# Kernel tuning notes

Hardware: AMD Instinct MI355X
Metric: run time of the kernel (lower is better)

Reference implementation:

```python
import jax, jax.numpy as jnp
import numpy as np
from jax import lax

VOCAB, VEC, HID, L, BATCH, OPT, K = 50000, 256, 256, 256, 8, 4, 2
H2, H8 = 2 * HID, 8 * HID


def _gru_dir(x, wih, whh, bih, bhh, reverse):
    # x: [B, L, D]; PyTorch GRU cell math.
    B = x.shape[0]
    H = whh.shape[1]
    def step(h, xt):
        gi = xt @ wih.T + bih            # [B, 3H]
        gh = h @ whh.T + bhh             # [B, 3H]
        ir, iz, inn = jnp.split(gi, 3, axis=-1)
        hr, hz, hn = jnp.split(gh, 3, axis=-1)
        r = jax.nn.sigmoid(ir + hr)
        z = jax.nn.sigmoid(iz + hz)
        n = jnp.tanh(inn + r * hn)
        hnew = (1.0 - z) * n + z * h
        return hnew, hnew
    h0 = jnp.zeros((B, H), x.dtype)
    _, ys = lax.scan(step, h0, jnp.swapaxes(x, 0, 1), reverse=reverse)
    return jnp.swapaxes(ys, 0, 1)        # [B, L, H]


def _bigru(x, wih, whh, bih, bhh):
    f = _gru_dir(x, wih[0], whh[0], bih[0], bhh[0], False)
    b = _gru_dir(x, wih[1], whh[1], bih[1], bhh[1], True)
    return jnp.concatenate([f, b], axis=-1)


def _bidaf(c, q, w, b):
    # s[b,i,j] = w_c.c_i + w_q.q_j + sum_d c_id*q_jd*w_cq_d + (b_c+b_q+b_cq)
    s = (c @ w[0])[:, :, None] + (q @ w[1])[:, None, :] \
        + jnp.einsum('bcd,bqd->bcq', c * w[2], q) + (b[0] + b[1] + b[2])
    a = jax.nn.softmax(s, axis=2)
    c2q = jnp.einsum('bcq,bqd->bcd', a, q)
    bb = jax.nn.softmax(jnp.max(s, axis=2), axis=1)        # [B, c_len]
    q2c = jnp.einsum('bc,bcd->bd', bb, c)[:, None, :]       # [B, 1, D]
    return jnp.concatenate([c, c2q, c * c2q, c * q2c], axis=-1)


def setup_inputs() -> dict:
    key = jax.random.key(0)
    ks = jax.random.split(key, 20)
    s = 0.05
    return {
        'question': jax.random.randint(ks[0], (BATCH, OPT, L), 0, VOCAB),
        'article': jax.random.randint(ks[1], (BATCH, OPT * K, L), 0, VOCAB),
        'emb': jax.random.normal(ks[2], (VOCAB, VEC), jnp.float32),
        'g1_wih': jax.random.normal(ks[3], (2, 3 * HID, VEC), jnp.float32) * s,
        'g1_whh': jax.random.normal(ks[4], (2, 3 * HID, HID), jnp.float32) * s,
        'g1_bih': jax.random.normal(ks[5], (2, 3 * HID), jnp.float32) * s,
        'g1_bhh': jax.random.normal(ks[6], (2, 3 * HID), jnp.float32) * s,
        'g2_wih': jax.random.normal(ks[7], (2, 3 * HID, H8), jnp.float32) * s,
        'g2_whh': jax.random.normal(ks[8], (2, 3 * HID, HID), jnp.float32) * s,
        'g2_bih': jax.random.normal(ks[9], (2, 3 * HID), jnp.float32) * s,
        'g2_bhh': jax.random.normal(ks[10], (2, 3 * HID), jnp.float32) * s,
        'b1_w': jax.random.normal(ks[11], (3, H2), jnp.float32) * s,
        'b1_b': jax.random.normal(ks[12], (3,), jnp.float32) * s,
        'b2_w': jax.random.normal(ks[13], (3, H2), jnp.float32) * s,
        'b2_b': jax.random.normal(ks[14], (3,), jnp.float32) * s,
        'rank_w': jax.random.normal(ks[15], (H8 * L,), jnp.float32) * 0.002,
        'rank_b': jax.random.normal(ks[16], (1,), jnp.float32) * s,
        'k': K,
        'option': OPT,
    }


def reference(question, article, emb, g1_wih, g1_whh, g1_bih, g1_bhh,
              g2_wih, g2_whh, g2_bih, g2_bhh, b1_w, b1_b, b2_w, b2_b,
              rank_w, rank_b, k, option):
    batch, _, max_len = question.shape
    # question.repeat(1,1,k).view(B*opt*k, L)
    q_ids = jnp.tile(question, (1, 1, k)).reshape(batch * option * k, max_len)
    a_ids = article.reshape(batch * option * k, max_len)
    qx = emb[q_ids]                                  # [Beff, L, VEC]
    ax = emb[a_ids]
    qh = _bigru(qx, g1_wih, g1_whh, g1_bih, g1_bhh)  # shared encoder, [Beff, L, 2H]
    ah = _bigru(ax, g1_wih, g1_whh, g1_bih, g1_bhh)
    att = jax.nn.relu(_bidaf(qh, ah, b1_w, b1_b))    # [Beff, L, 8H]
    ax2 = _bigru(att, g2_wih, g2_whh, g2_bih, g2_bhh)  # [Beff, L, 2H]
    ax2 = jax.nn.relu(_bidaf(ax2, ax2, b2_w, b2_b))    # [Beff, L, 8H]
    s = att + ax2
    # rank_method == 'max': max over k copies, then linear
    y = s.reshape(batch * option, k, -1)
    y = jnp.max(y, axis=1)                           # [B*opt, L*8H]
    y = y @ rank_w + rank_b[0]                       # [B*opt]
    return y.reshape(batch, option)
```

## Files before the change

### kernel.cpp

```cpp
#include <hip/hip_runtime.h>
#include <math.h>

#define LSEQ 256
#define HID 256
#define H2 512
#define H3 768
#define H8 2048

typedef __attribute__((ext_vector_type(8))) short short8;
typedef __attribute__((ext_vector_type(4))) float floatx4;

__device__ __forceinline__ unsigned short f2bf(float f) {
    unsigned int u = __float_as_uint(f);
    u = (u + 0x7FFFu + ((u >> 16) & 1u)) >> 16;
    return (unsigned short)u;
}
__device__ __forceinline__ float bf2f(unsigned short h) {
    return __uint_as_float(((unsigned int)h) << 16);
}
__device__ __forceinline__ float fsig(float x) {
    return __builtin_amdgcn_rcpf(1.f + __expf(-x));
}
__device__ __forceinline__ float ftanh(float x) {
    return __builtin_fmaf(2.f, __builtin_amdgcn_rcpf(1.f + __expf(-2.f * x)), -1.f);
}
__device__ __forceinline__ void bfsplit(float x, unsigned short& hi, unsigned short& lo) {
    hi = f2bf(x);
    lo = f2bf(x - bf2f(hi));
}

__global__ void embed_kernel(const int* __restrict__ question,
                             const int* __restrict__ article,
                             const float* __restrict__ emb,
                             unsigned short* __restrict__ xemb) {
    int gid = blockIdx.x * 256 + threadIdx.x;
    int d = gid & 255;
    int rl = gid >> 8;
    int l = rl & 255;
    int stream = rl >> 8;
    int id;
    if (stream < 64) {
        int b = stream >> 3, o = (stream & 7) >> 1;
        id = question[(b * 4 + o) * 256 + l];
    } else {
        id = article[(stream - 64) * 256 + l];
    }
    xemb[(size_t)gid] = f2bf(emb[(size_t)id * 256 + d]);
}

__global__ void pack_bf8(const float* __restrict__ src, unsigned short* __restrict__ dst, int n8) {
    int i = blockIdx.x * 256 + threadIdx.x;
    if (i >= n8) return;
    float4 a = ((const float4*)src)[2 * i];
    float4 b = ((const float4*)src)[2 * i + 1];
    uint4 o;
    o.x = (unsigned int)f2bf(a.x) | ((unsigned int)f2bf(a.y) << 16);
    o.y = (unsigned int)f2bf(a.z) | ((unsigned int)f2bf(a.w) << 16);
    o.z = (unsigned int)f2bf(b.x) | ((unsigned int)f2bf(b.y) << 16);
    o.w = (unsigned int)f2bf(b.z) | ((unsigned int)f2bf(b.w) << 16);
    ((uint4*)dst)[i] = o;
}

__global__ __launch_bounds__(256)
void gemm_a16b16(const unsigned short* __restrict__ A, const unsigned short* __restrict__ B,
                 const float* __restrict__ bias, unsigned short* __restrict__ C,
                 int M, int N, int K) {
    __shared__ unsigned short At[128][40];
    __shared__ unsigned short Bt[128][40];
    int tid = threadIdx.x;
    int m0 = blockIdx.x * 128, n0 = blockIdx.y * 128;
    int l = tid & 63, w = tid >> 6;
    int wm = (w & 1) * 64, wn = (w >> 1) * 64;
    int lr = l & 15, koff = (l >> 4) * 8;
    int srow = tid >> 1, scol = (tid & 1) * 16;
    floatx4 acc[4][4];
#pragma unroll
    for (int i = 0; i < 4; i++)
#pragma unroll
        for (int j = 0; j < 4; j++) acc[i][j] = (floatx4){0.f, 0.f, 0.f, 0.f};
    for (int k0 = 0; k0 < K; k0 += 32) {
        const unsigned short* ap = A + (size_t)(m0 + srow) * K + k0 + scol;
        const unsigned short* bp = B + (size_t)(n0 + srow) * K + k0 + scol;
        uint4 a0 = *(const uint4*)(ap);
        uint4 a1 = *(const uint4*)(ap + 8);
        uint4 b0 = *(const uint4*)(bp);
        uint4 b1 = *(const uint4*)(bp + 8);
        __syncthreads();
        *(uint4*)&At[srow][scol]     = a0;
        *(uint4*)&At[srow][scol + 8] = a1;
        *(uint4*)&Bt[srow][scol]     = b0;
        *(uint4*)&Bt[srow][scol + 8] = b1;
        __syncthreads();
        short8 af[4], bf[4];
#pragma unroll
        for (int i = 0; i < 4; i++) {
            af[i] = *(const short8*)&At[wm + i * 16 + lr][koff];
            bf[i] = *(const short8*)&Bt[wn + i * 16 + lr][koff];
        }
#pragma unroll
        for (int i = 0; i < 4; i++)
#pragma unroll
            for (int j = 0; j < 4; j++)
                acc[i][j] = __builtin_amdgcn_mfma_f32_16x16x32_bf16(af[i], bf[j], acc[i][j], 0, 0, 0);
    }
    int quad = l >> 4;
#pragma unroll
    for (int i = 0; i < 4; i++) {
#pragma unroll
        for (int j = 0; j < 4; j++) {
            int n = n0 + wn + j * 16 + lr;
            float bs = bias[n];
#pragma unroll
            for (int r = 0; r < 4; r++) {
                int m = m0 + wm + i * 16 + quad * 4 + r;
                C[(size_t)m * N + n] = f2bf(acc[i][j][r] + bs);
            }
        }
    }
}

__global__ __launch_bounds__(256)
void gemm_a32b16(const float* __restrict__ A, const unsigned short* __restrict__ B,
                 const float* __restrict__ bias, unsigned short* __restrict__ C,
                 int M, int N, int K) {
    __shared__ unsigned short At[128][40];
    __shared__ unsigned short Bt[128][40];
    int tid = threadIdx.x;
    int m0 = blockIdx.x * 128, n0 = blockIdx.y * 128;
    int l = tid & 63, w = tid >> 6;
    int wm = (w & 1) * 64, wn = (w >> 1) * 64;
    int lr = l & 15, koff = (l >> 4) * 8;
    int srow = tid >> 1, scol = (tid & 1) * 16;
    floatx4 acc[4][4];
#pragma unroll
    for (int i = 0; i < 4; i++)
#pragma unroll
        for (int j = 0; j < 4; j++) acc[i][j] = (floatx4){0.f, 0.f, 0.f, 0.f};
    for (int k0 = 0; k0 < K; k0 += 32) {
        const float* ap = A + (size_t)(m0 + srow) * K + k0 + scol;
        const unsigned short* bp = B + (size_t)(n0 + srow) * K + k0 + scol;
        float av[16];
        *(float4*)&av[0]  = *(const float4*)(ap);
        *(float4*)&av[4]  = *(const float4*)(ap + 4);
        *(float4*)&av[8]  = *(const float4*)(ap + 8);
        *(float4*)&av[12] = *(const float4*)(ap + 12);
        uint4 b0 = *(const uint4*)(bp);
        uint4 b1 = *(const uint4*)(bp + 8);
        unsigned int aw[8];
#pragma unroll
        for (int i = 0; i < 8; i++)
            aw[i] = (unsigned int)f2bf(av[2 * i]) | ((unsigned int)f2bf(av[2 * i + 1]) << 16);
        __syncthreads();
        *(uint4*)&At[srow][scol]     = *(uint4*)&aw[0];
        *(uint4*)&At[srow][scol + 8] = *(uint4*)&aw[4];
        *(uint4*)&Bt[srow][scol]     = b0;
        *(uint4*)&Bt[srow][scol + 8] = b1;
        __syncthreads();
        short8 af[4], bf[4];
#pragma unroll
        for (int i = 0; i < 4; i++) {
            af[i] = *(const short8*)&At[wm + i * 16 + lr][koff];
            bf[i] = *(const short8*)&Bt[wn + i * 16 + lr][koff];
        }
#pragma unroll
        for (int i = 0; i < 4; i++)
#pragma unroll
            for (int j = 0; j < 4; j++)
                acc[i][j] = __builtin_amdgcn_mfma_f32_16x16x32_bf16(af[i], bf[j], acc[i][j], 0, 0, 0);
    }
    int quad = l >> 4;
#pragma unroll
    for (int i = 0; i < 4; i++) {
#pragma unroll
        for (int j = 0; j < 4; j++) {
            int n = n0 + wn + j * 16 + lr;
            float bs = bias[n];
#pragma unroll
            for (int r = 0; r < 4; r++) {
                int m = m0 + wm + i * 16 + quad * 4 + r;
                C[(size_t)m * N + n] = f2bf(acc[i][j][r] + bs);
            }
        }
    }
}

__global__ __launch_bounds__(512, 2)
void gru_scan_rreg(const unsigned short* __restrict__ gi_f,
                   const unsigned short* __restrict__ gi_b,
                   const unsigned short* __restrict__ whh_bf,
                   const float* __restrict__ bhh,
                   float* __restrict__ out) {
    int blk = blockIdx.x;
    int d = blk & 1, s = blk >> 1;
    const unsigned short* gi_blk = (d ? gi_b : gi_f) + (size_t)s * LSEQ * H3;
    const unsigned short* wb = whh_bf + (size_t)d * H3 * HID;

    __shared__ __align__(16) unsigned short h_pack[2][256];

    int tid = threadIdx.x;
    int lane = tid & 63, wave = tid >> 6;
    int lr = lane & 15, kq = lane >> 4;

    short8 bq[6][8];
#pragma unroll
    for (int nt = 0; nt < 6; nt++) {
        int row = (nt >> 1) * 256 + wave * 32 + (nt & 1) * 16 + lr;
        const unsigned short* wp = wb + (size_t)row * HID + kq * 8;
#pragma unroll
        for (int kt = 0; kt < 8; kt++)
            bq[nt][kt] = *(const short8*)(wp + kt * 32);
    }

    int hh0 = wave * 32 + lr, hh1 = hh0 + 16;
    float br0 = bhh[d * H3 + hh0],       br1 = bhh[d * H3 + hh1];
    float bz0 = bhh[d * H3 + 256 + hh0], bz1 = bhh[d * H3 + 256 + hh1];
    float bn0 = bhh[d * H3 + 512 + hh0], bn1 = bhh[d * H3 + 512 + hh1];

    int t0 = d ? (LSEQ - 1) : 0;
    int tstep = d ? -1 : 1;

    if (tid < 128) ((unsigned int*)h_pack[0])[tid] = 0;
    float hold0 = 0.f, hold1 = 0.f;

    unsigned short gr0, gz0, gn0, gr1, gz1, gn1;
    {
        const unsigned short* gp = gi_blk + (size_t)t0 * H3;
        gr0 = gp[hh0]; gz0 = gp[256 + hh0]; gn0 = gp[512 + hh0];
        gr1 = gp[hh1]; gz1 = gp[256 + hh1]; gn1 = gp[512 + hh1];
    }
    __syncthreads();

    int cur = 0, t = t0;
    for (int step = 0; step < LSEQ; ++step) {
        unsigned short nr0 = 0, nz0 = 0, nn0 = 0, nr1 = 0, nz1 = 0, nn1 = 0;
        if (step + 1 < LSEQ) {
            const unsigned short* gp = gi_blk + (size_t)(t + tstep) * H3;
            nr0 = gp[hh0]; nz0 = gp[256 + hh0]; nn0 = gp[512 + hh0];
            nr1 = gp[hh1]; nz1 = gp[256 + hh1]; nn1 = gp[512 + hh1];
        }
        floatx4 acc[6];
#pragma unroll
        for (int nt = 0; nt < 6; nt++) acc[nt] = (floatx4){0.f, 0.f, 0.f, 0.f};
#pragma unroll
        for (int kt = 0; kt < 8; kt++) {
            short8 av = *(const short8*)&h_pack[cur][kt * 32 + kq * 8];
#pragma unroll
            for (int nt = 0; nt < 6; nt++)
                acc[nt] = __builtin_amdgcn_mfma_f32_16x16x32_bf16(av, bq[nt][kt], acc[nt], 0, 0, 0);
        }
        float rg0 = fsig(bf2f(gr0) + acc[0][0] + br0);
        float rg1 = fsig(bf2f(gr1) + acc[1][0] + br1);
        float zg0 = fsig(bf2f(gz0) + acc[2][0] + bz0);
        float zg1 = fsig(bf2f(gz1) + acc[3][0] + bz1);
        float ng0 = ftanh(bf2f(gn0) + rg0 * (acc[4][0] + bn0));
        float ng1 = ftanh(bf2f(gn1) + rg1 * (acc[5][0] + bn1));
        float h0 = (1.f - zg0) * ng0 + zg0 * hold0;
        float h1 = (1.f - zg1) * ng1 + zg1 * hold1;
        hold0 = h0; hold1 = h1;
        int nxt = cur ^ 1;
        if (kq == 0) {
            h_pack[nxt][hh0] = f2bf(h0);
            h_pack[nxt][hh1] = f2bf(h1);
            float* op = out + ((size_t)s * LSEQ + t) * H2 + d * HID;
            op[hh0] = h0;
            op[hh1] = h1;
        }
        gr0 = nr0; gz0 = nz0; gn0 = nn0;
        gr1 = nr1; gz1 = nz1; gn1 = nn1;
        __syncthreads();
        cur = nxt; t += tstep;
    }
}

__global__ void cwqw_kernel(const float* __restrict__ c, const float* __restrict__ q,
                            const float* __restrict__ w,
                            float* __restrict__ cw, float* __restrict__ qw) {
    int row = blockIdx.x;
    int lane = threadIdx.x;
    const float* src; const float* wv; float* dst; int r;
    if (row < 16384) { src = c; wv = w; dst = cw; r = row; }
    else { src = q; wv = w + 512; dst = qw; r = row - 16384; }
    const float* p = src + (size_t)r * H2;
    float acc = 0.f;
    for (int j = lane; j < H2; j += 64) acc += p[j] * wv[j];
    for (int off = 32; off; off >>= 1) acc += __shfl_down(acc, off);
    if (lane == 0) dst[r] = acc;
}

__global__ __launch_bounds__(256)
void smat_mfma(const float* __restrict__ c, const float* __restrict__ q,
               const float* __restrict__ w2, const float* __restrict__ bvec,
               const float* __restrict__ cw, const float* __restrict__ qw,
               float* __restrict__ smat) {
    __shared__ __align__(16) unsigned short Ah[128][40];
    __shared__ __align__(16) unsigned short Al[128][40];
    __shared__ __align__(16) unsigned short Bh[128][40];
    __shared__ __align__(16) unsigned short Bl[128][40];
    int b = blockIdx.z;
    int m0 = blockIdx.x * 128, n0 = blockIdx.y * 128;
    int tid = threadIdx.x;
    int l = tid & 63, w = tid >> 6;
    int wm = (w & 1) * 64, wn = (w >> 1) * 64;
    int lr = l & 15, koff = (l >> 4) * 8;
    int srow = tid >> 1, scol = (tid & 1) * 16;
    floatx4 acc[4][4];
#pragma unroll
    for (int i = 0; i < 4; i++)
#pragma unroll
        for (int j = 0; j < 4; j++) acc[i][j] = (floatx4){0.f, 0.f, 0.f, 0.f};
    const float* ap0 = c + (size_t)(b * 256 + m0 + srow) * H2 + scol;
    const float* bp0 = q + (size_t)(b * 256 + n0 + srow) * H2 + scol;
    for (int k0 = 0; k0 < H2; k0 += 32) {
        float av[16], bv[16], wv[16];
        *(float4*)&av[0]  = *(const float4*)(ap0 + k0);
        *(float4*)&av[4]  = *(const float4*)(ap0 + k0 + 4);
        *(float4*)&av[8]  = *(const float4*)(ap0 + k0 + 8);
        *(float4*)&av[12] = *(const float4*)(ap0 + k0 + 12);
        *(float4*)&bv[0]  = *(const float4*)(bp0 + k0);
        *(float4*)&bv[4]  = *(const float4*)(bp0 + k0 + 4);
        *(float4*)&bv[8]  = *(const float4*)(bp0 + k0 + 8);
        *(float4*)&bv[12] = *(const float4*)(bp0 + k0 + 12);
        *(float4*)&wv[0]  = *(const float4*)(w2 + k0 + scol);
        *(float4*)&wv[4]  = *(const float4*)(w2 + k0 + scol + 4);
        *(float4*)&wv[8]  = *(const float4*)(w2 + k0 + scol + 8);
        *(float4*)&wv[12] = *(const float4*)(w2 + k0 + scol + 12);
        unsigned int ahw[8], alw[8], bhw[8], blw[8];
#pragma unroll
        for (int j = 0; j < 8; j++) {
            float p0 = av[2 * j] * wv[2 * j], p1 = av[2 * j + 1] * wv[2 * j + 1];
            unsigned short h0, s0, h1, s1;
            bfsplit(p0, h0, s0); bfsplit(p1, h1, s1);
            ahw[j] = (unsigned int)h0 | ((unsigned int)h1 << 16);
            alw[j] = (unsigned int)s0 | ((unsigned int)s1 << 16);
            unsigned short g0, t0, g1, t1;
            bfsplit(bv[2 * j], g0, t0); bfsplit(bv[2 * j + 1], g1, t1);
            bhw[j] = (unsigned int)g0 | ((unsigned int)g1 << 16);
            blw[j] = (unsigned int)t0 | ((unsigned int)t1 << 16);
        }
        __syncthreads();
        *(uint4*)&Ah[srow][scol]     = *(uint4*)&ahw[0];
        *(uint4*)&Ah[srow][scol + 8] = *(uint4*)&ahw[4];
        *(uint4*)&Al[srow][scol]     = *(uint4*)&alw[0];
        *(uint4*)&Al[srow][scol + 8] = *(uint4*)&alw[4];
        *(uint4*)&Bh[srow][scol]     = *(uint4*)&bhw[0];
        *(uint4*)&Bh[srow][scol + 8] = *(uint4*)&bhw[4];
        *(uint4*)&Bl[srow][scol]     = *(uint4*)&blw[0];
        *(uint4*)&Bl[srow][scol + 8] = *(uint4*)&blw[4];
        __syncthreads();
        short8 afh[4], afl[4], bfh[4], bfl[4];
#pragma unroll
        for (int i = 0; i < 4; i++) {
            afh[i] = *(const short8*)&Ah[wm + i * 16 + lr][koff];
            afl[i] = *(const short8*)&Al[wm + i * 16 + lr][koff];
            bfh[i] = *(const short8*)&Bh[wn + i * 16 + lr][koff];
            bfl[i] = *(const short8*)&Bl[wn + i * 16 + lr][koff];
        }
#pragma unroll
        for (int i = 0; i < 4; i++)
#pragma unroll
            for (int j = 0; j < 4; j++) {
                acc[i][j] = __builtin_amdgcn_mfma_f32_16x16x32_bf16(afl[i], bfh[j], acc[i][j], 0, 0, 0);
                acc[i][j] = __builtin_amdgcn_mfma_f32_16x16x32_bf16(afh[i], bfl[j], acc[i][j], 0, 0, 0);
                acc[i][j] = __builtin_amdgcn_mfma_f32_16x16x32_bf16(afh[i], bfh[j], acc[i][j], 0, 0, 0);
            }
    }
    float bsum = bvec[0] + bvec[1] + bvec[2];
    int quad = l >> 4;
#pragma unroll
    for (int i = 0; i < 4; i++) {
#pragma unroll
        for (int j = 0; j < 4; j++) {
            int n = n0 + wn + j * 16 + lr;
            float qwv = qw[b * 256 + n] + bsum;
#pragma unroll
            for (int r = 0; r < 4; r++) {
                int m = m0 + wm + i * 16 + quad * 4 + r;
                smat[((size_t)(b * 256 + m)) * 256 + n] = acc[i][j][r] + cw[b * 256 + m] + qwv;
            }
        }
    }
}

__global__ void softmax_kernel(float* __restrict__ smat, float* __restrict__ rowmax) {
    int row = blockIdx.x;
    int lane = threadIdx.x;
    float* p = smat + (size_t)row * LSEQ;
    float v[4];
    float mx = -1e30f;
#pragma unroll
    for (int j = 0; j < 4; j++) { v[j] = p[lane + j * 64]; mx = fmaxf(mx, v[j]); }
    for (int off = 32; off; off >>= 1) mx = fmaxf(mx, __shfl_down(mx, off));
    mx = __shfl(mx, 0);
    float sum = 0.f;
#pragma unroll
    for (int j = 0; j < 4; j++) { v[j] = __expf(v[j] - mx); sum += v[j]; }
    for (int off = 32; off; off >>= 1) sum += __shfl_down(sum, off);
    sum = __shfl(sum, 0);
    float inv = 1.f / sum;
#pragma unroll
    for (int j = 0; j < 4; j++) p[lane + j * 64] = v[j] * inv;
    if (lane == 0) rowmax[row] = mx;
}

__global__ void bb_kernel(const float* __restrict__ rowmax, float* __restrict__ bb) {
    int b = blockIdx.x; int t = threadIdx.x;
    __shared__ float red[256];
    float v = rowmax[b * LSEQ + t];
    red[t] = v; __syncthreads();
    for (int s = 128; s; s >>= 1) { if (t < s) red[t] = fmaxf(red[t], red[t + s]); __syncthreads(); }
    float mx = red[0]; __syncthreads();
    float e = __expf(v - mx);
    red[t] = e; __syncthreads();
    for (int s = 128; s; s >>= 1) { if (t < s) red[t] += red[t + s]; __syncthreads(); }
    bb[b * LSEQ + t] = e / red[0];
}

__global__ void q2c_kernel(const float* __restrict__ bb, const float* __restrict__ c,
                           float* __restrict__ q2c) {
    int b = blockIdx.x;
    int d = blockIdx.y * 128 + threadIdx.x;
    const float* cb = c + (size_t)b * LSEQ * H2 + d;
    const float* bbp = bb + b * LSEQ;
    float a0 = 0.f, a1 = 0.f, a2 = 0.f, a3 = 0.f;
    for (int i = 0; i < LSEQ; i += 4) {
        a0 += bbp[i]     * cb[(size_t)i * H2];
        a1 += bbp[i + 1] * cb[(size_t)(i + 1) * H2];
        a2 += bbp[i + 2] * cb[(size_t)(i + 2) * H2];
        a3 += bbp[i + 3] * cb[(size_t)(i + 3) * H2];
    }
    q2c[b * H2 + d] = (a0 + a1) + (a2 + a3);
}

__global__ __launch_bounds__(256)
void c2q_mfma(const float* __restrict__ amat, const float* __restrict__ q,
              const float* __restrict__ c, float* __restrict__ att, int add) {
    __shared__ __align__(16) unsigned short Ah[128][40];
    __shared__ __align__(16) unsigned short Al[128][40];
    __shared__ __align__(16) unsigned short Bh[128][40];
    __shared__ __align__(16) unsigned short Bl[128][40];
    int b = blockIdx.z;
    int m0 = blockIdx.x * 128, n0 = blockIdx.y * 128;
    int tid = threadIdx.x;
    int l = tid & 63, w = tid >> 6;
    int wm = (w & 1) * 64, wn = (w >> 1) * 64;
    int lr = l & 15, koff = (l >> 4) * 8;
    int srow = tid >> 1, scol = (tid & 1) * 16;
    int bn = tid & 127, bkh = tid >> 7;
    floatx4 acc[4][4];
#pragma unroll
    for (int i = 0; i < 4; i++)
#pragma unroll
        for (int j = 0; j < 4; j++) acc[i][j] = (floatx4){0.f, 0.f, 0.f, 0.f};
    for (int k0 = 0; k0 < LSEQ; k0 += 32) {
        float av[16];
        const float* ap = amat + (size_t)(b * 256 + m0 + srow) * 256 + k0 + scol;
        *(float4*)&av[0]  = *(const float4*)(ap);
        *(float4*)&av[4]  = *(const float4*)(ap + 4);
        *(float4*)&av[8]  = *(const float4*)(ap + 8);
        *(float4*)&av[12] = *(const float4*)(ap + 12);
        float qv[16];
        const float* qp = q + (size_t)(b * 256 + k0 + bkh * 16) * H2 + n0 + bn;
#pragma unroll
        for (int j = 0; j < 16; j++) qv[j] = qp[(size_t)j * H2];
        unsigned int ahw[8], alw[8], bhw[8], blw[8];
#pragma unroll
        for (int j = 0; j < 8; j++) {
            unsigned short h0, s0, h1, s1;
            bfsplit(av[2 * j], h0, s0); bfsplit(av[2 * j + 1], h1, s1);
            ahw[j] = (unsigned int)h0 | ((unsigned int)h1 << 16);
            alw[j] = (unsigned int)s0 | ((unsigned int)s1 << 16);
            unsigned short g0, t0, g1, t1;
            bfsplit(qv[2 * j], g0, t0); bfsplit(qv[2 * j + 1], g1, t1);
            bhw[j] = (unsigned int)g0 | ((unsigned int)g1 << 16);
            blw[j] = (unsigned int)t0 | ((unsigned int)t1 << 16);
        }
        __syncthreads();
        *(uint4*)&Ah[srow][scol]         = *(uint4*)&ahw[0];
        *(uint4*)&Ah[srow][scol + 8]     = *(uint4*)&ahw[4];
        *(uint4*)&Al[srow][scol]         = *(uint4*)&alw[0];
        *(uint4*)&Al[srow][scol + 8]     = *(uint4*)&alw[4];
        *(uint4*)&Bh[bn][bkh * 16]       = *(uint4*)&bhw[0];
        *(uint4*)&Bh[bn][bkh * 16 + 8]   = *(uint4*)&bhw[4];
        *(uint4*)&Bl[bn][bkh * 16]       = *(uint4*)&blw[0];
        *(uint4*)&Bl[bn][bkh * 16 + 8]   = *(uint4*)&blw[4];
        __syncthreads();
        short8 afh[4], afl[4], bfh[4], bfl[4];
#pragma unroll
        for (int i = 0; i < 4; i++) {
            afh[i] = *(const short8*)&Ah[wm + i * 16 + lr][koff];
            afl[i] = *(const short8*)&Al[wm + i * 16 + lr][koff];
            bfh[i] = *(const short8*)&Bh[wn + i * 16 + lr][koff];
            bfl[i] = *(const short8*)&Bl[wn + i * 16 + lr][koff];
        }
#pragma unroll
        for (int i = 0; i < 4; i++)
#pragma unroll
            for (int j = 0; j < 4; j++) {
                acc[i][j] = __builtin_amdgcn_mfma_f32_16x16x32_bf16(afl[i], bfh[j], acc[i][j], 0, 0, 0);
                acc[i][j] = __builtin_amdgcn_mfma_f32_16x16x32_bf16(afh[i], bfl[j], acc[i][j], 0, 0, 0);
                acc[i][j] = __builtin_amdgcn_mfma_f32_16x16x32_bf16(afh[i], bfh[j], acc[i][j], 0, 0, 0);
            }
    }
    int quad = l >> 4;
#pragma unroll
    for (int i = 0; i < 4; i++) {
#pragma unroll
        for (int j = 0; j < 4; j++) {
            int n = n0 + wn + j * 16 + lr;
#pragma unroll
            for (int r = 0; r < 4; r++) {
                int m = m0 + wm + i * 16 + quad * 4 + r;
                size_t row = (size_t)b * 256 + m;
                float a = acc[i][j][r];
                float cv = c[row * H2 + n];
                float v1 = fmaxf(a, 0.f);
                float v2 = fmaxf(cv * a, 0.f);
                float* p1 = att + row * H8 + 512 + n;
                float* p2 = att + row * H8 + 1024 + n;
                if (add) { *p1 += v1; *p2 += v2; }
                else     { *p1 = v1;  *p2 = v2; }
            }
        }
    }
}

__global__ void fixup03(const float* __restrict__ c, const float* __restrict__ q2c,
                        float* __restrict__ att, int add) {
    int row = blockIdx.x;
    int t = threadIdx.x;
    int b = row >> 8;
    float* o = att + (size_t)row * H8;
#pragma unroll
    for (int rep = 0; rep < 2; rep++) {
        int d = t + rep * 256;
        float cv = c[(size_t)row * H2 + d];
        float qv = q2c[b * H2 + d];
        float v0 = fmaxf(cv, 0.f);
        float v3 = fmaxf(cv * qv, 0.f);
        if (add) { o[d] += v0; o[d + 1536] += v3; }
        else     { o[d]  = v0; o[d + 1536]  = v3; }
    }
}

__global__ void reduce1_kernel(const float* __restrict__ s, const float* __restrict__ rw,
                               float* __restrict__ part) {
    int bo = blockIdx.x;
    int p = blockIdx.y;
    int t = threadIdx.x;
    const float* s0 = s + (size_t)(2 * bo) * 524288;
    const float* s1 = s0 + 524288;
    size_t base = (size_t)p * 65536;
    float acc = 0.f;
    for (int j = t; j < 65536; j += 256) {
        size_t m = base + j;
        acc += rw[m] * fmaxf(s0[m], s1[m]);
    }
    __shared__ float red[256];
    red[t] = acc; __syncthreads();
    for (int ss = 128; ss; ss >>= 1) { if (t < ss) red[t] += red[t + ss]; __syncthreads(); }
    if (t == 0) part[bo * 8 + p] = red[0];
}

__global__ void reduce2_kernel(const float* __restrict__ part, const float* __restrict__ rb,
                               float* __restrict__ out) {
    int t = threadIdx.x;
    float a = rb[0];
    for (int p = 0; p < 8; p++) a += part[t * 8 + p];
    out[t] = a;
}

extern "C" void kernel_launch(void* const* d_in, const int* in_sizes, int n_in,
                              void* d_out, int out_size, void* d_ws, size_t ws_size,
                              hipStream_t stream) {
    const int* question = (const int*)d_in[0];
    const int* article  = (const int*)d_in[1];
    const float* emb    = (const float*)d_in[2];
    const float* g1_wih = (const float*)d_in[3];
    const float* g1_whh = (const float*)d_in[4];
    const float* g1_bih = (const float*)d_in[5];
    const float* g1_bhh = (const float*)d_in[6];
    const float* g2_wih = (const float*)d_in[7];
    const float* g2_whh = (const float*)d_in[8];
    const float* g2_bih = (const float*)d_in[9];
    const float* g2_bhh = (const float*)d_in[10];
    const float* b1_w   = (const float*)d_in[11];
    const float* b1_b   = (const float*)d_in[12];
    const float* b2_w   = (const float*)d_in[13];
    const float* b2_b   = (const float*)d_in[14];
    const float* rank_w = (const float*)d_in[15];
    const float* rank_b = (const float*)d_in[16];
    float* ws = (float*)d_ws;
    float* out = (float*)d_out;

    unsigned short* WPK1  = (unsigned short*)(ws);
    unsigned short* WIH1B = (unsigned short*)(ws + 196608);
    unsigned short* WPK2  = (unsigned short*)(ws + 393216);
    unsigned short* WIH2B = (unsigned short*)(ws + 589824);
    float* CW   = ws + 2162688;
    float* QW   = ws + 2179072;
    float* RM   = ws + 2195456;
    float* BBv  = ws + 2211840;
    float* Q2C  = ws + 2228224;
    float* PART = ws + 2260992;
    unsigned short* XEMBB = (unsigned short*)(ws + 2293760);
    float*          SMAT  = ws + 2293760;
    unsigned short* GI2B  = (unsigned short*)(ws + 2293760);
    float*          HBUF  = ws + 6488064;
    float*          AX2   = ws + 14876672;
    float*          ATT   = ws + 25165824;
    unsigned short* GI1B  = (unsigned short*)(ws + 25165824);

    embed_kernel<<<32768, 256, 0, stream>>>(question, article, emb, XEMBB);
    pack_bf8<<<192, 256, 0, stream>>>(g1_whh, WPK1, 49152);
    pack_bf8<<<192, 256, 0, stream>>>(g1_wih, WIH1B, 49152);
    pack_bf8<<<192, 256, 0, stream>>>(g2_whh, WPK2, 49152);
    pack_bf8<<<1536, 256, 0, stream>>>(g2_wih, WIH2B, 393216);

    for (int d = 0; d < 2; d++) {
        gemm_a16b16<<<dim3(256, 6), 256, 0, stream>>>(
            XEMBB, WIH1B + (size_t)d * 196608, g1_bih + d * 768,
            GI1B + (size_t)d * 25165824, 32768, 768, 256);
    }
    gru_scan_rreg<<<256, 512, 0, stream>>>(GI1B, GI1B + (size_t)25165824, WPK1, g1_bhh, HBUF);

    float* QH = HBUF;
    float* AH = HBUF + (size_t)64 * 256 * 512;

    {
        cwqw_kernel<<<32768, 64, 0, stream>>>(QH, AH, b1_w, CW, QW);
        smat_mfma<<<dim3(2, 2, 64), 256, 0, stream>>>(QH, AH, b1_w + 1024, b1_b, CW, QW, SMAT);
        softmax_kernel<<<16384, 64, 0, stream>>>(SMAT, RM);
        bb_kernel<<<64, 256, 0, stream>>>(RM, BBv);
        q2c_kernel<<<dim3(64, 4), 128, 0, stream>>>(BBv, QH, Q2C);
        fixup03<<<16384, 256, 0, stream>>>(QH, Q2C, ATT, 0);
        c2q_mfma<<<dim3(2, 4, 64), 256, 0, stream>>>(SMAT, AH, QH, ATT, 0);
    }

    for (int d = 0; d < 2; d++) {
        gemm_a32b16<<<dim3(128, 6), 256, 0, stream>>>(
            ATT, WIH2B + (size_t)d * 1572864, g2_bih + d * 768,
            GI2B + (size_t)d * 12582912, 16384, 768, 2048);
    }
    gru_scan_rreg<<<128, 512, 0, stream>>>(GI2B, GI2B + (size_t)12582912, WPK2, g2_bhh, AX2);

    {
        cwqw_kernel<<<32768, 64, 0, stream>>>(AX2, AX2, b2_w, CW, QW);
        smat_mfma<<<dim3(2, 2, 64), 256, 0, stream>>>(AX2, AX2, b2_w + 1024, b2_b, CW, QW, SMAT);
        softmax_kernel<<<16384, 64, 0, stream>>>(SMAT, RM);
        bb_kernel<<<64, 256, 0, stream>>>(RM, BBv);
        q2c_kernel<<<dim3(64, 4), 128, 0, stream>>>(BBv, AX2, Q2C);
        fixup03<<<16384, 256, 0, stream>>>(AX2, Q2C, ATT, 1);
        c2q_mfma<<<dim3(2, 4, 64), 256, 0, stream>>>(SMAT, AX2, AX2, ATT, 1);
    }

    reduce1_kernel<<<dim3(32, 8), 256, 0, stream>>>(ATT, rank_w, PART);
    reduce2_kernel<<<1, 32, 0, stream>>>(PART, rank_b, out);
}
```

Before: 1.399 ms.

## Merge direction GEMMs, fuse fixup into c2q epilogue, pre-pack ATT to bf16

```diff
diff --git a/kernel.cpp b/kernel.cpp
--- a/kernel.cpp
+++ b/kernel.cpp
@@ -62,9 +62,9 @@
 }
 
 __global__ __launch_bounds__(256)
-void gemm_a16b16(const unsigned short* __restrict__ A, const unsigned short* __restrict__ B,
-                 const float* __restrict__ bias, unsigned short* __restrict__ C,
-                 int M, int N, int K) {
+void gemm_2dir(const unsigned short* __restrict__ A, const unsigned short* __restrict__ B,
+               const float* __restrict__ bias, unsigned short* __restrict__ C0,
+               unsigned short* __restrict__ C1, int mbase, int K) {
     __shared__ unsigned short At[128][40];
     __shared__ unsigned short Bt[128][40];
     int tid = threadIdx.x;
@@ -110,75 +110,12 @@
         for (int j = 0; j < 4; j++) {
             int n = n0 + wn + j * 16 + lr;
             float bs = bias[n];
+            unsigned short* dst = (n < 768) ? C0 : C1;
+            int nn = (n < 768) ? n : n - 768;
 #pragma unroll
             for (int r = 0; r < 4; r++) {
-                int m = m0 + wm + i * 16 + quad * 4 + r;
-                C[(size_t)m * N + n] = f2bf(acc[i][j][r] + bs);
-            }
-        }
-    }
-}
-
-__global__ __launch_bounds__(256)
-void gemm_a32b16(const float* __restrict__ A, const unsigned short* __restrict__ B,
-                 const float* __restrict__ bias, unsigned short* __restrict__ C,
-                 int M, int N, int K) {
-    __shared__ unsigned short At[128][40];
-    __shared__ unsigned short Bt[128][40];
-    int tid = threadIdx.x;
-    int m0 = blockIdx.x * 128, n0 = blockIdx.y * 128;
-    int l = tid & 63, w = tid >> 6;
-    int wm = (w & 1) * 64, wn = (w >> 1) * 64;
-    int lr = l & 15, koff = (l >> 4) * 8;
-    int srow = tid >> 1, scol = (tid & 1) * 16;
-    floatx4 acc[4][4];
-#pragma unroll
-    for (int i = 0; i < 4; i++)
-#pragma unroll
-        for (int j = 0; j < 4; j++) acc[i][j] = (floatx4){0.f, 0.f, 0.f, 0.f};
-    for (int k0 = 0; k0 < K; k0 += 32) {
-        const float* ap = A + (size_t)(m0 + srow) * K + k0 + scol;
-        const unsigned short* bp = B + (size_t)(n0 + srow) * K + k0 + scol;
-        float av[16];
-        *(float4*)&av[0]  = *(const float4*)(ap);
-        *(float4*)&av[4]  = *(const float4*)(ap + 4);
-        *(float4*)&av[8]  = *(const float4*)(ap + 8);
-        *(float4*)&av[12] = *(const float4*)(ap + 12);
-        uint4 b0 = *(const uint4*)(bp);
-        uint4 b1 = *(const uint4*)(bp + 8);
-        unsigned int aw[8];
-#pragma unroll
-        for (int i = 0; i < 8; i++)
-            aw[i] = (unsigned int)f2bf(av[2 * i]) | ((unsigned int)f2bf(av[2 * i + 1]) << 16);
-        __syncthreads();
-        *(uint4*)&At[srow][scol]     = *(uint4*)&aw[0];
-        *(uint4*)&At[srow][scol + 8] = *(uint4*)&aw[4];
-        *(uint4*)&Bt[srow][scol]     = b0;
-        *(uint4*)&Bt[srow][scol + 8] = b1;
-        __syncthreads();
-        short8 af[4], bf[4];
-#pragma unroll
-        for (int i = 0; i < 4; i++) {
-            af[i] = *(const short8*)&At[wm + i * 16 + lr][koff];
-            bf[i] = *(const short8*)&Bt[wn + i * 16 + lr][koff];
-        }
-#pragma unroll
-        for (int i = 0; i < 4; i++)
-#pragma unroll
-            for (int j = 0; j < 4; j++)
-                acc[i][j] = __builtin_amdgcn_mfma_f32_16x16x32_bf16(af[i], bf[j], acc[i][j], 0, 0, 0);
-    }
-    int quad = l >> 4;
-#pragma unroll
-    for (int i = 0; i < 4; i++) {
-#pragma unroll
-        for (int j = 0; j < 4; j++) {
-            int n = n0 + wn + j * 16 + lr;
-            float bs = bias[n];
-#pragma unroll
-            for (int r = 0; r < 4; r++) {
-                int m = m0 + wm + i * 16 + quad * 4 + r;
-                C[(size_t)m * N + n] = f2bf(acc[i][j][r] + bs);
+                int m = mbase + m0 + wm + i * 16 + quad * 4 + r;
+                dst[(size_t)m * 768 + nn] = f2bf(acc[i][j][r] + bs);
             }
         }
     }
@@ -432,8 +369,9 @@
 }
 
 __global__ __launch_bounds__(256)
-void c2q_mfma(const float* __restrict__ amat, const float* __restrict__ q,
-              const float* __restrict__ c, float* __restrict__ att, int add) {
+void c2q_fix_mfma(const float* __restrict__ amat, const float* __restrict__ q,
+                  const float* __restrict__ c, const float* __restrict__ q2c,
+                  float* __restrict__ att, int add) {
     __shared__ __align__(16) unsigned short Ah[128][40];
     __shared__ __align__(16) unsigned short Al[128][40];
     __shared__ __align__(16) unsigned short Bh[128][40];
@@ -507,38 +445,25 @@
 #pragma unroll
         for (int j = 0; j < 4; j++) {
             int n = n0 + wn + j * 16 + lr;
+            float q2cv = q2c[b * H2 + n];
 #pragma unroll
             for (int r = 0; r < 4; r++) {
                 int m = m0 + wm + i * 16 + quad * 4 + r;
                 size_t row = (size_t)b * 256 + m;
                 float a = acc[i][j][r];
                 float cv = c[row * H2 + n];
+                float v0 = fmaxf(cv, 0.f);
                 float v1 = fmaxf(a, 0.f);
                 float v2 = fmaxf(cv * a, 0.f);
-                float* p1 = att + row * H8 + 512 + n;
-                float* p2 = att + row * H8 + 1024 + n;
-                if (add) { *p1 += v1; *p2 += v2; }
-                else     { *p1 = v1;  *p2 = v2; }
+                float v3 = fmaxf(cv * q2cv, 0.f);
+                float* p0 = att + row * H8 + n;
+                float* p1 = p0 + 512;
+                float* p2 = p0 + 1024;
+                float* p3 = p0 + 1536;
+                if (add) { *p0 += v0; *p1 += v1; *p2 += v2; *p3 += v3; }
+                else     { *p0 = v0;  *p1 = v1;  *p2 = v2;  *p3 = v3; }
             }
         }
-    }
-}
-
-__global__ void fixup03(const float* __restrict__ c, const float* __restrict__ q2c,
-                        float* __restrict__ att, int add) {
-    int row = blockIdx.x;
-    int t = threadIdx.x;
-    int b = row >> 8;
-    float* o = att + (size_t)row * H8;
-#pragma unroll
-    for (int rep = 0; rep < 2; rep++) {
-        int d = t + rep * 256;
-        float cv = c[(size_t)row * H2 + d];
-        float qv = q2c[b * H2 + d];
-        float v0 = fmaxf(cv, 0.f);
-        float v3 = fmaxf(cv * qv, 0.f);
-        if (add) { o[d] += v0; o[d + 1536] += v3; }
-        else     { o[d]  = v0; o[d + 1536]  = v3; }
     }
 }
 
@@ -606,6 +531,7 @@
     float*          SMAT  = ws + 2293760;
     unsigned short* GI2B  = (unsigned short*)(ws + 2293760);
     float*          HBUF  = ws + 6488064;
+    unsigned short* ATTBH = (unsigned short*)(ws + 14876672);
     float*          AX2   = ws + 14876672;
     float*          ATT   = ws + 25165824;
     unsigned short* GI1B  = (unsigned short*)(ws + 25165824);
@@ -616,11 +542,8 @@
     pack_bf8<<<192, 256, 0, stream>>>(g2_whh, WPK2, 49152);
     pack_bf8<<<1536, 256, 0, stream>>>(g2_wih, WIH2B, 393216);
 
-    for (int d = 0; d < 2; d++) {
-        gemm_a16b16<<<dim3(256, 6), 256, 0, stream>>>(
-            XEMBB, WIH1B + (size_t)d * 196608, g1_bih + d * 768,
-            GI1B + (size_t)d * 25165824, 32768, 768, 256);
-    }
+    gemm_2dir<<<dim3(256, 12), 256, 0, stream>>>(
+        XEMBB, WIH1B, g1_bih, GI1B, GI1B + (size_t)25165824, 0, 256);
     gru_scan_rreg<<<256, 512, 0, stream>>>(GI1B, GI1B + (size_t)25165824, WPK1, g1_bhh, HBUF);
 
     float* QH = HBUF;
@@ -632,14 +555,13 @@
         softmax_kernel<<<16384, 64, 0, stream>>>(SMAT, RM);
         bb_kernel<<<64, 256, 0, stream>>>(RM, BBv);
         q2c_kernel<<<dim3(64, 4), 128, 0, stream>>>(BBv, QH, Q2C);
-        fixup03<<<16384, 256, 0, stream>>>(QH, Q2C, ATT, 0);
-        c2q_mfma<<<dim3(2, 4, 64), 256, 0, stream>>>(SMAT, AH, QH, ATT, 0);
-    }
-
-    for (int d = 0; d < 2; d++) {
-        gemm_a32b16<<<dim3(128, 6), 256, 0, stream>>>(
-            ATT, WIH2B + (size_t)d * 1572864, g2_bih + d * 768,
-            GI2B + (size_t)d * 12582912, 16384, 768, 2048);
+        c2q_fix_mfma<<<dim3(2, 4, 64), 256, 0, stream>>>(SMAT, AH, QH, Q2C, ATT, 0);
+    }
+
+    for (int half = 0; half < 2; half++) {
+        pack_bf8<<<8192, 256, 0, stream>>>(ATT + (size_t)half * 16777216, ATTBH, 2097152);
+        gemm_2dir<<<dim3(64, 12), 256, 0, stream>>>(
+            ATTBH, WIH2B, g2_bih, GI2B, GI2B + (size_t)12582912, half * 8192, 2048);
     }
     gru_scan_rreg<<<128, 512, 0, stream>>>(GI2B, GI2B + (size_t)12582912, WPK2, g2_bhh, AX2);
 
@@ -649,8 +571,7 @@
         softmax_kernel<<<16384, 64, 0, stream>>>(SMAT, RM);
         bb_kernel<<<64, 256, 0, stream>>>(RM, BBv);
         q2c_kernel<<<dim3(64, 4), 128, 0, stream>>>(BBv, AX2, Q2C);
-        fixup03<<<16384, 256, 0, stream>>>(AX2, Q2C, ATT, 1);
-        c2q_mfma<<<dim3(2, 4, 64), 256, 0, stream>>>(SMAT, AX2, AX2, ATT, 1);
+        c2q_fix_mfma<<<dim3(2, 4, 64), 256, 0, stream>>>(SMAT, AX2, AX2, Q2C, ATT, 1);
     }
 
     reduce1_kernel<<<dim3(32, 8), 256, 0, stream>>>(ATT, rank_w, PART);
```

New measurement: 1.360 ms. 1.03x faster.
